# Optimization experiments

Measured on AMD Instinct MI355X. Metric: run time of the kernel, lower is better.

Reference implementation:

```python
import jax, jax.numpy as jnp
import numpy as np

HEADS = 4
C = 128            # per-head out channels (hard-coded 128 in the module)
NEG_SLOPE_ATT = 0.2   # GATConv attention leaky_relu slope
NEG_SLOPE = 0.01      # F.leaky_relu default slope


def _diag_output_ids(num_groups, n):
    # ids = base_i + n*j + j for group i, agent j; base_i = i * n^2
    i = np.arange(num_groups)[:, None] * (n * n)
    j = np.arange(n)[None, :] * (n + 1)
    return jnp.asarray((i + j).reshape(-1))


def setup_inputs() -> dict:
    key = jax.random.key(0)
    ks = jax.random.split(key, 12)
    num_groups, n_agents = 12, 48
    N = num_groups * n_agents * n_agents      # 27648 nodes
    E = 442368
    F_in, edge_dim, hidden = 256, 16, 256
    s = 0.05
    return {
        "x": jax.random.normal(ks[0], (N, F_in), jnp.float32),
        "edge_index": jax.random.randint(ks[1], (2, E), 0, N, jnp.int32),
        "edge_attr": jax.random.normal(ks[2], (E, edge_dim), jnp.float32),
        "num_groups": num_groups,
        "agents_per_group": n_agents,
        "W": jax.random.normal(ks[3], (F_in, HEADS * C), jnp.float32) * s,
        "att_src": jax.random.normal(ks[4], (HEADS, C), jnp.float32) * s,
        "att_dst": jax.random.normal(ks[5], (HEADS, C), jnp.float32) * s,
        "W_edge": jax.random.normal(ks[6], (edge_dim, HEADS * C), jnp.float32) * s,
        "att_edge": jax.random.normal(ks[7], (HEADS, C), jnp.float32) * s,
        "bias_gat": jnp.zeros((HEADS * C,), jnp.float32),
        "fc_W": jax.random.normal(ks[8], (HEADS * C, hidden), jnp.float32) * s,
        "fc_b": jnp.zeros((hidden,), jnp.float32),
    }


def _gat_conv(x, src, dst, edge_attr_full, W, att_src, att_dst, W_edge, att_edge, bias):
    N = x.shape[0]
    h = (x @ W).reshape(N, HEADS, C)                       # [N,H,C]
    a_src = jnp.einsum('nhc,hc->nh', h, att_src)           # [N,H]
    a_dst = jnp.einsum('nhc,hc->nh', h, att_dst)
    he = (edge_attr_full @ W_edge).reshape(-1, HEADS, C)   # [E',H,C]
    a_edge = jnp.einsum('ehc,hc->eh', he, att_edge)
    logits = jax.nn.leaky_relu(a_src[src] + a_dst[dst] + a_edge, NEG_SLOPE_ATT)
    # segment softmax over incoming edges of each dst node
    m = jax.ops.segment_max(logits, dst, num_segments=N)   # [N,H]
    e = jnp.exp(logits - m[dst])
    s = jax.ops.segment_sum(e, dst, num_segments=N)
    alpha = e / (s[dst] + 1e-16)                           # [E',H]
    msg = h[src] * alpha[..., None]                        # [E',H,C]
    out = jax.ops.segment_sum(msg, dst, num_segments=N)    # [N,H,C]
    return out.reshape(N, HEADS * C) + bias


def reference(x, edge_index, edge_attr, num_groups, agents_per_group,
              W, att_src, att_dst, W_edge, att_edge, bias_gat, fc_W, fc_b):
    N = x.shape[0]
    # add self-loops (PyG default), self-loop edge_attr = mean fill
    loops = jnp.arange(N, dtype=edge_index.dtype)
    src = jnp.concatenate([edge_index[0], loops])
    dst = jnp.concatenate([edge_index[1], loops])
    ea = jnp.concatenate([edge_attr,
                          jnp.broadcast_to(edge_attr.mean(0), (N, edge_attr.shape[1]))])
    h = jax.nn.leaky_relu(
        _gat_conv(x, src, dst, ea, W, att_src, att_dst, W_edge, att_edge, bias_gat),
        NEG_SLOPE)
    ids = _diag_output_ids(num_groups, agents_per_group)
    # fc_output + leaky_relu then diagonal index-select (select first: same math)
    return jax.nn.leaky_relu(h[ids] @ fc_W + fc_b, NEG_SLOPE)
```

## Files before the change

### kernel.cpp

```cpp
#include <hip/hip_runtime.h>

#define NNODES 27648
#define NEDGES 442368
#define FIN    256
#define HC     512
#define NH     4
#define CDIM   128
#define NAG    48
#define NGRP   12
#define N2     2304
#define NOUT   576
#define CAP    128
#define EDIM   16
#define MPART  512


__device__ __forceinline__ float lrelu(float v, float s){ return v > 0.0f ? v : s * v; }

__device__ __forceinline__ float wsum(float v){
  #pragma unroll
  for (int off = 32; off; off >>= 1) v += __shfl_xor(v, off, 64);
  return v;
}
__device__ __forceinline__ float wmax(float v){
  #pragma unroll
  for (int off = 32; off; off >>= 1) v = fmaxf(v, __shfl_xor(v, off, 64));
  return v;
}

__global__ __launch_bounds__(256) void k_pre(
    const float* __restrict__ W, const float* __restrict__ att_src,
    const float* __restrict__ att_dst, const float* __restrict__ W_edge,
    const float* __restrict__ att_edge, const float* __restrict__ ea,
    float* __restrict__ ws_, float* __restrict__ wd_, float* __restrict__ we_,
    int* __restrict__ counts, float4* __restrict__ easum_part){
  int b = blockIdx.x;
  int tid = threadIdx.x;
  if (b < 11) {
    int g = b * 256 + tid;
    if (g < 1024) {
      int f = g >> 2, h = g & 3;
      const float4* wp = (const float4*)(W + f*HC + h*CDIM);
      const float4* ap = (const float4*)(att_src + h*CDIM);
      float s = 0.f;
      #pragma unroll 8
      for (int c4 = 0; c4 < CDIM/4; c4++){
        float4 wv = wp[c4], av = ap[c4];
        s += wv.x*av.x + wv.y*av.y + wv.z*av.z + wv.w*av.w;
      }
      ws_[g] = s;
    } else if (g < 2048) {
      int gg = g - 1024; int f = gg >> 2, h = gg & 3;
      const float4* wp = (const float4*)(W + f*HC + h*CDIM);
      const float4* ap = (const float4*)(att_dst + h*CDIM);
      float s = 0.f;
      #pragma unroll 8
      for (int c4 = 0; c4 < CDIM/4; c4++){
        float4 wv = wp[c4], av = ap[c4];
        s += wv.x*av.x + wv.y*av.y + wv.z*av.z + wv.w*av.w;
      }
      wd_[gg] = s;
    } else if (g < 2112) {
      int gg = g - 2048; int d = gg >> 2, h = gg & 3;
      const float4* wp = (const float4*)(W_edge + d*HC + h*CDIM);
      const float4* ap = (const float4*)(att_edge + h*CDIM);
      float s = 0.f;
      #pragma unroll 8
      for (int c4 = 0; c4 < CDIM/4; c4++){
        float4 wv = wp[c4], av = ap[c4];
        s += wv.x*av.x + wv.y*av.y + wv.z*av.z + wv.w*av.w;
      }
      we_[gg] = s;
    } else if (g < 2112 + NOUT) {
      counts[g - 2112] = 0;
    }
  } else {
    int pb = b - 11;
    const float4* p = (const float4*)ea;
    const int total = NEDGES * 4;
    float4 acc = make_float4(0.f, 0.f, 0.f, 0.f);
    for (int i = pb*256 + tid; i < total; i += MPART*256){
      float4 v = p[i];
      acc.x += v.x; acc.y += v.y; acc.z += v.z; acc.w += v.w;
    }
    #pragma unroll
    for (int off = 4; off <= 32; off <<= 1){
      acc.x += __shfl_xor(acc.x, off, 64);
      acc.y += __shfl_xor(acc.y, off, 64);
      acc.z += __shfl_xor(acc.z, off, 64);
      acc.w += __shfl_xor(acc.w, off, 64);
    }
    __shared__ float4 sd4[16];
    int lane = tid & 63, wave = tid >> 6;
    if (lane < 4) sd4[wave*4 + lane] = acc;
    __syncthreads();
    if (tid < 4){
      float4 t = sd4[tid];
      float4 a = sd4[4+tid], c = sd4[8+tid], d = sd4[12+tid];
      t.x += a.x + c.x + d.x; t.y += a.y + c.y + d.y;
      t.z += a.z + c.z + d.z; t.w += a.w + c.w + d.w;
      easum_part[pb*4 + tid] = t;
    }
  }
}

__global__ __launch_bounds__(256) void k_scan(const int* __restrict__ ei,
    const float* __restrict__ ea, const float* __restrict__ we_,
    int* __restrict__ counts, int* __restrict__ slist, float* __restrict__ aed,
    const float* __restrict__ easum_part, float* __restrict__ easum){
  int tid = threadIdx.x;
  if (blockIdx.x == NEDGES/256){
    int col = tid & 15, part = tid >> 4;
    float s = 0.f;
    for (int pb = 0; pb < MPART/16; pb++)
      s += easum_part[(part*(MPART/16) + pb)*16 + col];
    __shared__ float sd[256];
    sd[tid] = s;
    __syncthreads();
    if (tid < 16){
      float t = 0.f;
      #pragma unroll
      for (int i = 0; i < 16; i++) t += sd[i*16 + tid];
      easum[tid] = t;
    }
    return;
  }
  int e = blockIdx.x*256 + tid;
  int dst = ei[NEDGES + e];
  int r = dst % N2;
  if (r % 49) return;
  int row = (dst / N2) * NAG + r / 49;
  int pos = atomicAdd(&counts[row], 1);
  if (pos >= CAP) return;
  slist[row*CAP + pos] = ei[e];
  const float* eap = ea + (size_t)e*EDIM;
  float a0=0.f,a1=0.f,a2=0.f,a3=0.f;
  #pragma unroll
  for (int d = 0; d < EDIM; d++){
    float v = eap[d];
    a0 += v*we_[d*4+0]; a1 += v*we_[d*4+1]; a2 += v*we_[d*4+2]; a3 += v*we_[d*4+3];
  }
  float* ap = aed + (size_t)(row*CAP+pos)*4;
  ap[0]=a0; ap[1]=a1; ap[2]=a2; ap[3]=a3;
}

__global__ __launch_bounds__(512) void k_mega(const float* __restrict__ x,
    const float* __restrict__ ws_, const float* __restrict__ wd_,
    const float* __restrict__ we_, const float* __restrict__ easum,
    const int* __restrict__ counts, const int* __restrict__ slist,
    const float* __restrict__ aed,
    const float* __restrict__ W, const float* __restrict__ bias,
    const float* __restrict__ fcW, const float* __restrict__ fcb,
    float* __restrict__ out){
  __shared__ float  lg[2][(CAP+1)*4];
  __shared__ int    srcs[2][CAP+1];
  __shared__ float  adst[2][4];
  __shared__ float4 zs4[2][256];
  __shared__ float  hsf[2][512];
  __shared__ float4 scratch[2048];
  int rowA = blockIdx.x * 2;
  int tid = threadIdx.x;
  int lane = tid & 63, wave = tid >> 6;
  int rsel = wave >> 2;
  int w4 = wave & 3;

  int kA = counts[rowA];     if (kA > CAP) kA = CAP;
  int kB = counts[rowA + 1]; if (kB > CAP) kB = CAP;
  int myRow = rowA + rsel;
  int myK = rsel ? kB : kA;
  int gg = myRow / NAG, jj = myRow - gg*NAG;
  int myDst = gg*N2 + jj*49;

  float wsr[4][4];
  #pragma unroll
  for (int q = 0; q < 4; q++){
    float4 t = *(const float4*)(ws_ + (lane*4+q)*4);
    wsr[q][0]=t.x; wsr[q][1]=t.y; wsr[q][2]=t.z; wsr[q][3]=t.w;
  }

  for (int i = w4; i < myK; i += 4){
    int src = slist[myRow*CAP + i];
    float4 aedv = *(const float4*)(aed + (size_t)(myRow*CAP+i)*4);
    float4 xv = *(const float4*)(x + (size_t)src*FIN + lane*4);
    float p0 = xv.x*wsr[0][0] + xv.y*wsr[1][0] + xv.z*wsr[2][0] + xv.w*wsr[3][0];
    float p1 = xv.x*wsr[0][1] + xv.y*wsr[1][1] + xv.z*wsr[2][1] + xv.w*wsr[3][1];
    float p2 = xv.x*wsr[0][2] + xv.y*wsr[1][2] + xv.z*wsr[2][2] + xv.w*wsr[3][2];
    float p3 = xv.x*wsr[0][3] + xv.y*wsr[1][3] + xv.z*wsr[2][3] + xv.w*wsr[3][3];
    p0 = wsum(p0); p1 = wsum(p1); p2 = wsum(p2); p3 = wsum(p3);
    if (lane == 0){
      srcs[rsel][i] = src;
      lg[rsel][i*4+0] = p0 + aedv.x; lg[rsel][i*4+1] = p1 + aedv.y;
      lg[rsel][i*4+2] = p2 + aedv.z; lg[rsel][i*4+3] = p3 + aedv.w;
    }
  }

  if (w4 == 0){
    float wdr[4][4];
    #pragma unroll
    for (int q = 0; q < 4; q++){
      float4 t = *(const float4*)(wd_ + (lane*4+q)*4);
      wdr[q][0]=t.x; wdr[q][1]=t.y; wdr[q][2]=t.z; wdr[q][3]=t.w;
    }
    float4 xv = *(const float4*)(x + (size_t)myDst*FIN + lane*4);
    float pd[4], ps[4];
    #pragma unroll
    for (int h = 0; h < 4; h++){
      pd[h] = xv.x*wdr[0][h] + xv.y*wdr[1][h] + xv.z*wdr[2][h] + xv.w*wdr[3][h];
      ps[h] = xv.x*wsr[0][h] + xv.y*wsr[1][h] + xv.z*wsr[2][h] + xv.w*wsr[3][h];
    }
    const float invE = 1.0f/(float)NEDGES;
    float md = (lane < 16) ? easum[lane]*invE : 0.f;
    float al[4];
    #pragma unroll
    for (int h = 0; h < 4; h++){
      float c = (lane < 16) ? md*we_[lane*4+h] : 0.f;
      al[h] = wsum(c);
      pd[h] = wsum(pd[h]);
      ps[h] = wsum(ps[h]);
    }
    if (lane == 0){
      #pragma unroll
      for (int h = 0; h < 4; h++){
        adst[rsel][h] = pd[h];
        lg[rsel][myK*4+h] = ps[h] + al[h];
      }
      srcs[rsel][myK] = myDst;
    }
  }
  __syncthreads();

  {
    int r = wave >> 2, h = wave & 3;
    int kk = r ? kB : kA;
    float ad = adst[r][h];
    float m = -1e30f;
    for (int i = lane; i <= kk; i += 64){
      float v = lrelu(lg[r][i*4+h] + ad, 0.2f);
      lg[r][i*4+h] = v;
      m = fmaxf(m, v);
    }
    m = wmax(m);
    float s = 0.f;
    for (int i = lane; i <= kk; i += 64){
      float e = __expf(lg[r][i*4+h] - m);
      lg[r][i*4+h] = e;
      s += e;
    }
    s = wsum(s);
    float inv = 1.0f/(s + 1e-16f);
    for (int i = lane; i <= kk; i += 64) lg[r][i*4+h] *= inv;
  }
  __syncthreads();

  {
    float acc[4][4];
    #pragma unroll
    for (int h = 0; h < 4; h++)
      #pragma unroll
      for (int c = 0; c < 4; c++) acc[h][c] = 0.f;
    for (int i = w4; i <= myK; i += 4){
      int src = srcs[rsel][i];
      float4 xv = *(const float4*)(x + (size_t)src*FIN + lane*4);
      float a0 = lg[rsel][i*4+0], a1 = lg[rsel][i*4+1];
      float a2 = lg[rsel][i*4+2], a3 = lg[rsel][i*4+3];
      acc[0][0] += a0*xv.x; acc[0][1] += a0*xv.y; acc[0][2] += a0*xv.z; acc[0][3] += a0*xv.w;
      acc[1][0] += a1*xv.x; acc[1][1] += a1*xv.y; acc[1][2] += a1*xv.z; acc[1][3] += a1*xv.w;
      acc[2][0] += a2*xv.x; acc[2][1] += a2*xv.y; acc[2][2] += a2*xv.z; acc[2][3] += a2*xv.w;
      acc[3][0] += a3*xv.x; acc[3][1] += a3*xv.y; acc[3][2] += a3*xv.z; acc[3][3] += a3*xv.w;
    }
    #pragma unroll
    for (int h = 0; h < 4; h++)
      scratch[rsel*1024 + w4*256 + h*64 + lane] =
        make_float4(acc[h][0], acc[h][1], acc[h][2], acc[h][3]);
  }
  __syncthreads();
  {
    int r = tid >> 8, s = tid & 255;
    float4 a = scratch[r*1024 + 0*256 + s], b = scratch[r*1024 + 1*256 + s];
    float4 c = scratch[r*1024 + 2*256 + s], d = scratch[r*1024 + 3*256 + s];
    zs4[r][s] = make_float4(a.x+b.x+c.x+d.x, a.y+b.y+c.y+d.y,
                            a.z+b.z+c.z+d.z, a.w+b.w+c.w+d.w);
  }
  __syncthreads();

  {
    int cg = tid & 127;
    int q  = tid >> 7;
    int h  = cg >> 5;
    const float* zA = (const float*)&zs4[0][0] + h*256 + q*64;
    const float* zB = (const float*)&zs4[1][0] + h*256 + q*64;
    const float4* Wp = (const float4*)(W + (size_t)q*64*HC) + cg;
    float4 aA = make_float4(0.f,0.f,0.f,0.f);
    float4 aB = make_float4(0.f,0.f,0.f,0.f);
    #pragma unroll 8
    for (int r = 0; r < 64; r++){
      float4 w4v = Wp[(size_t)r*(HC/4)];
      float za = zA[r], zb = zB[r];
      aA.x += za*w4v.x; aA.y += za*w4v.y; aA.z += za*w4v.z; aA.w += za*w4v.w;
      aB.x += zb*w4v.x; aB.y += zb*w4v.y; aB.z += zb*w4v.z; aB.w += zb*w4v.w;
    }
    scratch[0*512 + q*128 + cg] = aA;
    scratch[1*512 + q*128 + cg] = aB;
  }
  __syncthreads();
  if (tid < 256){
    int r = tid >> 7, cg = tid & 127;
    float4 a = scratch[r*512 + 0*128 + cg], b = scratch[r*512 + 1*128 + cg];
    float4 c = scratch[r*512 + 2*128 + cg], d = scratch[r*512 + 3*128 + cg];
    float4 bs = ((const float4*)bias)[cg];
    hsf[r][4*cg+0] = lrelu(a.x+b.x+c.x+d.x+bs.x, 0.01f);
    hsf[r][4*cg+1] = lrelu(a.y+b.y+c.y+d.y+bs.y, 0.01f);
    hsf[r][4*cg+2] = lrelu(a.z+b.z+c.z+d.z+bs.z, 0.01f);
    hsf[r][4*cg+3] = lrelu(a.w+b.w+c.w+d.w+bs.w, 0.01f);
  }
  __syncthreads();

  {
    int cg = tid & 63;
    int e  = tid >> 6;
    const float4* Fp = (const float4*)(fcW + (size_t)e*64*256) + cg;
    const float* hA = &hsf[0][0] + e*64;
    const float* hB = &hsf[1][0] + e*64;
    float4 aA = make_float4(0.f,0.f,0.f,0.f);
    float4 aB = make_float4(0.f,0.f,0.f,0.f);
    #pragma unroll 8
    for (int r = 0; r < 64; r++){
      float4 w4v = Fp[(size_t)r*64];
      float ha = hA[r], hb = hB[r];
      aA.x += ha*w4v.x; aA.y += ha*w4v.y; aA.z += ha*w4v.z; aA.w += ha*w4v.w;
      aB.x += hb*w4v.x; aB.y += hb*w4v.y; aB.z += hb*w4v.z; aB.w += hb*w4v.w;
    }
    scratch[0*512 + e*64 + cg] = aA;
    scratch[1*512 + e*64 + cg] = aB;
  }
  __syncthreads();
  if (tid < 128){
    int r = tid >> 6, cg = tid & 63;
    float4 s0 = scratch[r*512 + 0*64 + cg];
    #pragma unroll
    for (int e = 1; e < 8; e++){
      float4 t = scratch[r*512 + e*64 + cg];
      s0.x += t.x; s0.y += t.y; s0.z += t.z; s0.w += t.w;
    }
    float4 bs = ((const float4*)fcb)[cg];
    float4 o;
    o.x = lrelu(s0.x+bs.x, 0.01f);
    o.y = lrelu(s0.y+bs.y, 0.01f);
    o.z = lrelu(s0.z+bs.z, 0.01f);
    o.w = lrelu(s0.w+bs.w, 0.01f);
    *(float4*)(out + (size_t)(rowA + r)*256 + 4*cg) = o;
  }
}

extern "C" void kernel_launch(void* const* d_in, const int* in_sizes, int n_in,
                              void* d_out, int out_size, void* d_ws, size_t ws_size,
                              hipStream_t stream) {
  const float* x        = (const float*)d_in[0];
  const int*   ei       = (const int*)  d_in[1];
  const float* ea       = (const float*)d_in[2];
  const float* W        = (const float*)d_in[5];
  const float* att_src  = (const float*)d_in[6];
  const float* att_dst  = (const float*)d_in[7];
  const float* W_edge   = (const float*)d_in[8];
  const float* att_edge = (const float*)d_in[9];
  const float* bias     = (const float*)d_in[10];
  const float* fcW      = (const float*)d_in[11];
  const float* fcb      = (const float*)d_in[12];
  float* out = (float*)d_out;

  float* w = (float*)d_ws;
  float*  ws_       = w;
  float*  wd_       = w + 1024;
  float*  we_       = w + 2048;
  float*  easum     = w + 2112;
  int*    counts    = (int*)(w + 2128);
  float*  easum_p   = w + 2704;
  int*    slist     = (int*)(w + 10896);
  float*  aed       = w + 84624;

  k_pre<<<11 + MPART, 256, 0, stream>>>(W, att_src, att_dst, W_edge, att_edge, ea,
                                        ws_, wd_, we_, counts, (float4*)easum_p);
  k_scan<<<NEDGES/256 + 1, 256, 0, stream>>>(ei, ea, we_, counts, slist, aed,
                                             easum_p, easum);
  k_mega<<<NOUT/2, 512, 0, stream>>>(x, ws_, wd_, we_, easum, counts, slist, aed,
                                     W, bias, fcW, fcb, out);
}
```

Before: 149.6 us.

## Precompute per-node attention scores for all nodes in scan kernel

Moves the per-source attention projection (x·ws and x·wd) out of the mega kernel into extra blocks of the scan kernel, which compute a_src/a_dst for every node once. The mega kernel then builds logits by gathering small float4 scores instead of reading 1KB feature rows and doing wave reductions per edge, and the self-loop edge term is precomputed once. The trade-off is computing scores for all 27648 nodes (reading all of x, about 28MB) rather than only the gathered sources.

Measured after the change: 153.7 us. +2.7%, slower.

```diff
diff --git a/kernel.cpp b/kernel.cpp
--- a/kernel.cpp
+++ b/kernel.cpp
@@ -13,6 +13,8 @@
 #define CAP    128
 #define EDIM   16
 #define MPART  512
+#define SCANB  (NEDGES/256)
+#define ASRCB0 (SCANB + 1)
 
 
 __device__ __forceinline__ float lrelu(float v, float s){ return v > 0.0f ? v : s * v; }
@@ -106,15 +108,40 @@
 
 __global__ __launch_bounds__(256) void k_scan(const int* __restrict__ ei,
     const float* __restrict__ ea, const float* __restrict__ we_,
+    const float* __restrict__ ws_, const float* __restrict__ wd_,
+    const float* __restrict__ x,
     int* __restrict__ counts, int* __restrict__ slist, float* __restrict__ aed,
-    const float* __restrict__ easum_part, float* __restrict__ easum){
+    const float* __restrict__ easum_part, float* __restrict__ easum,
+    float* __restrict__ mal, float* __restrict__ asrc, float* __restrict__ adst){
   int tid = threadIdx.x;
-  if (blockIdx.x == NEDGES/256){
+  int b = blockIdx.x;
+  if (b < SCANB){
+    int e = b*256 + tid;
+    int dst = ei[NEDGES + e];
+    int r = dst % N2;
+    if (r % 49) return;
+    int row = (dst / N2) * NAG + r / 49;
+    int pos = atomicAdd(&counts[row], 1);
+    if (pos >= CAP) return;
+    slist[row*CAP + pos] = ei[e];
+    const float* eap = ea + (size_t)e*EDIM;
+    float a0=0.f,a1=0.f,a2=0.f,a3=0.f;
+    #pragma unroll
+    for (int d = 0; d < EDIM; d++){
+      float v = eap[d];
+      a0 += v*we_[d*4+0]; a1 += v*we_[d*4+1]; a2 += v*we_[d*4+2]; a3 += v*we_[d*4+3];
+    }
+    float* ap = aed + (size_t)(row*CAP+pos)*4;
+    ap[0]=a0; ap[1]=a1; ap[2]=a2; ap[3]=a3;
+    return;
+  }
+  if (b == SCANB){
     int col = tid & 15, part = tid >> 4;
     float s = 0.f;
     for (int pb = 0; pb < MPART/16; pb++)
       s += easum_part[(part*(MPART/16) + pb)*16 + col];
     __shared__ float sd[256];
+    __shared__ float se[16];
     sd[tid] = s;
     __syncthreads();
     if (tid < 16){
@@ -122,31 +149,43 @@
       #pragma unroll
       for (int i = 0; i < 16; i++) t += sd[i*16 + tid];
       easum[tid] = t;
+      se[tid] = t;
+    }
+    __syncthreads();
+    if (tid < 4){
+      const float invE = 1.0f/(float)NEDGES;
+      float m = 0.f;
+      #pragma unroll
+      for (int d = 0; d < 16; d++) m += se[d]*invE*we_[d*4+tid];
+      mal[tid] = m;
     }
     return;
   }
-  int e = blockIdx.x*256 + tid;
-  int dst = ei[NEDGES + e];
-  int r = dst % N2;
-  if (r % 49) return;
-  int row = (dst / N2) * NAG + r / 49;
-  int pos = atomicAdd(&counts[row], 1);
-  if (pos >= CAP) return;
-  slist[row*CAP + pos] = ei[e];
-  const float* eap = ea + (size_t)e*EDIM;
-  float a0=0.f,a1=0.f,a2=0.f,a3=0.f;
-  #pragma unroll
-  for (int d = 0; d < EDIM; d++){
-    float v = eap[d];
-    a0 += v*we_[d*4+0]; a1 += v*we_[d*4+1]; a2 += v*we_[d*4+2]; a3 += v*we_[d*4+3];
-  }
-  float* ap = aed + (size_t)(row*CAP+pos)*4;
-  ap[0]=a0; ap[1]=a1; ap[2]=a2; ap[3]=a3;
+  {
+    int lane = tid & 63, wave = tid >> 6;
+    int node = (b - ASRCB0)*4 + wave;
+    float4 xv = *(const float4*)(x + (size_t)node*FIN + lane*4);
+    float ps[4] = {0.f,0.f,0.f,0.f}, pd[4] = {0.f,0.f,0.f,0.f};
+    #pragma unroll
+    for (int q = 0; q < 4; q++){
+      float4 wsv = *(const float4*)(ws_ + (lane*4+q)*4);
+      float4 wdv = *(const float4*)(wd_ + (lane*4+q)*4);
+      float xq = (q==0) ? xv.x : (q==1) ? xv.y : (q==2) ? xv.z : xv.w;
+      ps[0]+=xq*wsv.x; ps[1]+=xq*wsv.y; ps[2]+=xq*wsv.z; ps[3]+=xq*wsv.w;
+      pd[0]+=xq*wdv.x; pd[1]+=xq*wdv.y; pd[2]+=xq*wdv.z; pd[3]+=xq*wdv.w;
+    }
+    #pragma unroll
+    for (int h = 0; h < 4; h++){ ps[h] = wsum(ps[h]); pd[h] = wsum(pd[h]); }
+    if (lane == 0){
+      *(float4*)(asrc + (size_t)node*4) = make_float4(ps[0],ps[1],ps[2],ps[3]);
+      *(float4*)(adst + (size_t)node*4) = make_float4(pd[0],pd[1],pd[2],pd[3]);
+    }
+  }
 }
 
 __global__ __launch_bounds__(512) void k_mega(const float* __restrict__ x,
-    const float* __restrict__ ws_, const float* __restrict__ wd_,
-    const float* __restrict__ we_, const float* __restrict__ easum,
+    const float* __restrict__ asrc, const float* __restrict__ adst,
+    const float* __restrict__ mal,
     const int* __restrict__ counts, const int* __restrict__ slist,
     const float* __restrict__ aed,
     const float* __restrict__ W, const float* __restrict__ bias,
@@ -154,7 +193,6 @@
     float* __restrict__ out){
   __shared__ float  lg[2][(CAP+1)*4];
   __shared__ int    srcs[2][CAP+1];
-  __shared__ float  adst[2][4];
   __shared__ float4 zs4[2][256];
   __shared__ float  hsf[2][512];
   __shared__ float4 scratch[2048];
@@ -166,65 +204,33 @@
 
   int kA = counts[rowA];     if (kA > CAP) kA = CAP;
   int kB = counts[rowA + 1]; if (kB > CAP) kB = CAP;
-  int myRow = rowA + rsel;
-  int myK = rsel ? kB : kA;
-  int gg = myRow / NAG, jj = myRow - gg*NAG;
-  int myDst = gg*N2 + jj*49;
-
-  float wsr[4][4];
-  #pragma unroll
-  for (int q = 0; q < 4; q++){
-    float4 t = *(const float4*)(ws_ + (lane*4+q)*4);
-    wsr[q][0]=t.x; wsr[q][1]=t.y; wsr[q][2]=t.z; wsr[q][3]=t.w;
-  }
-
-  for (int i = w4; i < myK; i += 4){
-    int src = slist[myRow*CAP + i];
-    float4 aedv = *(const float4*)(aed + (size_t)(myRow*CAP+i)*4);
-    float4 xv = *(const float4*)(x + (size_t)src*FIN + lane*4);
-    float p0 = xv.x*wsr[0][0] + xv.y*wsr[1][0] + xv.z*wsr[2][0] + xv.w*wsr[3][0];
-    float p1 = xv.x*wsr[0][1] + xv.y*wsr[1][1] + xv.z*wsr[2][1] + xv.w*wsr[3][1];
-    float p2 = xv.x*wsr[0][2] + xv.y*wsr[1][2] + xv.z*wsr[2][2] + xv.w*wsr[3][2];
-    float p3 = xv.x*wsr[0][3] + xv.y*wsr[1][3] + xv.z*wsr[2][3] + xv.w*wsr[3][3];
-    p0 = wsum(p0); p1 = wsum(p1); p2 = wsum(p2); p3 = wsum(p3);
-    if (lane == 0){
-      srcs[rsel][i] = src;
-      lg[rsel][i*4+0] = p0 + aedv.x; lg[rsel][i*4+1] = p1 + aedv.y;
-      lg[rsel][i*4+2] = p2 + aedv.z; lg[rsel][i*4+3] = p3 + aedv.w;
-    }
-  }
-
-  if (w4 == 0){
-    float wdr[4][4];
-    #pragma unroll
-    for (int q = 0; q < 4; q++){
-      float4 t = *(const float4*)(wd_ + (lane*4+q)*4);
-      wdr[q][0]=t.x; wdr[q][1]=t.y; wdr[q][2]=t.z; wdr[q][3]=t.w;
-    }
-    float4 xv = *(const float4*)(x + (size_t)myDst*FIN + lane*4);
-    float pd[4], ps[4];
-    #pragma unroll
-    for (int h = 0; h < 4; h++){
-      pd[h] = xv.x*wdr[0][h] + xv.y*wdr[1][h] + xv.z*wdr[2][h] + xv.w*wdr[3][h];
-      ps[h] = xv.x*wsr[0][h] + xv.y*wsr[1][h] + xv.z*wsr[2][h] + xv.w*wsr[3][h];
-    }
-    const float invE = 1.0f/(float)NEDGES;
-    float md = (lane < 16) ? easum[lane]*invE : 0.f;
-    float al[4];
-    #pragma unroll
-    for (int h = 0; h < 4; h++){
-      float c = (lane < 16) ? md*we_[lane*4+h] : 0.f;
-      al[h] = wsum(c);
-      pd[h] = wsum(pd[h]);
-      ps[h] = wsum(ps[h]);
-    }
-    if (lane == 0){
-      #pragma unroll
-      for (int h = 0; h < 4; h++){
-        adst[rsel][h] = pd[h];
-        lg[rsel][myK*4+h] = ps[h] + al[h];
+  int gA = rowA / NAG,  jA = rowA - gA*NAG;
+  int dstA = gA*N2 + jA*49;
+  int gB = (rowA+1) / NAG, jB = (rowA+1) - gB*NAG;
+  int dstB = gB*N2 + jB*49;
+
+  {
+    int r = tid >> 8;
+    int i = tid & 255;
+    int kk = r ? kB : kA;
+    int drow = r ? dstB : dstA;
+    if (i <= kk){
+      int row = rowA + r;
+      int src; float4 aedv;
+      if (i < kk){
+        src = slist[row*CAP + i];
+        aedv = *(const float4*)(aed + (size_t)(row*CAP+i)*4);
+      } else {
+        src = drow;
+        aedv = *(const float4*)mal;
       }
-      srcs[rsel][myK] = myDst;
+      float4 as = *(const float4*)(asrc + (size_t)src*4);
+      float4 ad = *(const float4*)(adst + (size_t)drow*4);
+      srcs[r][i] = src;
+      lg[r][i*4+0] = lrelu(as.x + ad.x + aedv.x, 0.2f);
+      lg[r][i*4+1] = lrelu(as.y + ad.y + aedv.y, 0.2f);
+      lg[r][i*4+2] = lrelu(as.z + ad.z + aedv.z, 0.2f);
+      lg[r][i*4+3] = lrelu(as.w + ad.w + aedv.w, 0.2f);
     }
   }
   __syncthreads();
@@ -232,13 +238,8 @@
   {
     int r = wave >> 2, h = wave & 3;
     int kk = r ? kB : kA;
-    float ad = adst[r][h];
     float m = -1e30f;
-    for (int i = lane; i <= kk; i += 64){
-      float v = lrelu(lg[r][i*4+h] + ad, 0.2f);
-      lg[r][i*4+h] = v;
-      m = fmaxf(m, v);
-    }
+    for (int i = lane; i <= kk; i += 64) m = fmaxf(m, lg[r][i*4+h]);
     m = wmax(m);
     float s = 0.f;
     for (int i = lane; i <= kk; i += 64){
@@ -253,6 +254,7 @@
   __syncthreads();
 
   {
+    int myK = rsel ? kB : kA;
     float acc[4][4];
     #pragma unroll
     for (int h = 0; h < 4; h++)
@@ -377,11 +379,15 @@
   float*  easum_p   = w + 2704;
   int*    slist     = (int*)(w + 10896);
   float*  aed       = w + 84624;
+  float*  asrc      = w + 379536;
+  float*  adst      = w + 490128;
+  float*  mal       = w + 600720;
 
   k_pre<<<11 + MPART, 256, 0, stream>>>(W, att_src, att_dst, W_edge, att_edge, ea,
                                         ws_, wd_, we_, counts, (float4*)easum_p);
-  k_scan<<<NEDGES/256 + 1, 256, 0, stream>>>(ei, ea, we_, counts, slist, aed,
-                                             easum_p, easum);
-  k_mega<<<NOUT/2, 512, 0, stream>>>(x, ws_, wd_, we_, easum, counts, slist, aed,
+  k_scan<<<ASRCB0 + NNODES/4, 256, 0, stream>>>(ei, ea, we_, ws_, wd_, x,
+                                                counts, slist, aed,
+                                                easum_p, easum, mal, asrc, adst);
+  k_mega<<<NOUT/2, 512, 0, stream>>>(x, asrc, adst, mal, counts, slist, aed,
                                      W, bias, fcW, fcb, out);
 }
```
